# Optimization experiments

Measured on AMD Instinct MI355X. Metric: run time of the kernel, lower is better.

Reference implementation:

```python
import jax, jax.numpy as jnp
import numpy as np

# ---- fixed configuration (from init_kwargs / sensor='WV3', ratio=4) ----
B, NBANDS, H, W = 4, 8, 512, 512
RATIO = 4
BETA = 0.25
KSIZE = 41                    # MTF kernel size used by gen_mtf
SCALE = 2                     # ceil(ratio / 2), StructuralLoss half-window
MASK_HW = 8                   # half-window used by local_corr_mask
MTF_R = MTF_C = 2             # strided scatter offsets in SpectralLossNocorr
EPS = 1e-20
# WV3 Nyquist gains (one per MS band)
GNYQ = np.asarray([0.325, 0.355, 0.360, 0.350, 0.365, 0.360, 0.335, 0.315])


def gen_mtf_kernel():
    """Per-band Gaussian MTF filter, shape (NBANDS, 1, K, K), sum-normalized."""
    fcut = 1.0 / RATIO
    ax = np.arange(KSIZE) - (KSIZE - 1) / 2.0
    xx, yy = np.meshgrid(ax, ax)
    kerns = []
    for g in GNYQ:
        alpha = np.sqrt(((KSIZE - 1) * (fcut / 2.0)) ** 2 / (-2.0 * np.log(g)))
        k = np.exp(-(xx ** 2 + yy ** 2) / (2.0 * alpha ** 2))
        kerns.append(k / k.sum())
    return np.stack(kerns, axis=0)[:, None].astype(np.float32)


def _boxsum(x, w):
    """Sum over a 2w x 2w sliding window via double cumsum (matches torch ref)."""
    x = jnp.pad(x, ((0, 0), (0, 0), (w, w), (w, w)))
    c = jnp.cumsum(jnp.cumsum(x, axis=-1), axis=-2)
    return (c[..., 2 * w:, 2 * w:] - c[..., :-2 * w, 2 * w:]
            - c[..., 2 * w:, :-2 * w] + c[..., :-2 * w, :-2 * w])


def _xcorr(a, b, w):
    """Local cross-correlation (xcorr_torch). a:(B,Ca,H,W), b:(B,Cb,H,W) broadcast."""
    n = 4.0 * w * w
    da = a - _boxsum(a, w) / n
    db = b - _boxsum(b, w) / n
    s_ab = _boxsum(da * db, w)
    s_aa = _boxsum(da * da, w)
    s_bb = _boxsum(db * db, w)
    return s_ab / (jnp.sqrt(s_aa * s_bb) + EPS)


def _depthconv(x, kern):
    # torch Conv2d(groups=nbands, padding='same') == grouped cross-correlation
    return jax.lax.conv_general_dilated(
        x, kern, (1, 1), 'SAME', feature_group_count=kern.shape[0],
        dimension_numbers=('NCHW', 'OIHW', 'NCHW'))


def _local_corr_mask(inp, kern):
    pan = inp[:, -1:, :, :]          # (B,1,H,W)
    ms = inp[:, :-1, :, :]           # (B,NB,H,W)
    k0 = kern[0:1]                   # first-band MTF kernel (1,1,K,K)
    pad = (KSIZE - 1) // 2
    pan = jnp.pad(pan, ((0, 0), (0, 0), (pad, pad), (pad, pad)), mode='edge')
    pan = jax.lax.conv_general_dilated(
        pan, k0, (1, 1), 'VALID', dimension_numbers=('NCHW', 'OIHW', 'NCHW'))
    return 1.0 - _xcorr(pan, ms, MASK_HW)  # (B,NB,H,W)


def setup_inputs() -> dict:
    key = jax.random.key(0)
    k1, k2, k3 = jax.random.split(key, 3)
    return {
        'outputs': jax.random.normal(k1, (B, NBANDS, H, W), jnp.float32),
        'labels': jax.random.uniform(k2, (B, NBANDS + 1, H, W), jnp.float32),
        'inp': jax.random.uniform(k3, (B, NBANDS + 1, H, W), jnp.float32),
        'mtf_kernel': jnp.asarray(gen_mtf_kernel()),           # frozen param
        'spec_mask': jnp.ones((1, NBANDS, H, W), jnp.float32),  # buffer
    }


def reference(outputs, labels, inp, mtf_kernel, spec_mask):
    # ---- SpectralLossNocorr ----
    x = _depthconv(outputs, mtf_kernel)                      # (B,NB,H,W)
    labels_spec = labels[:, :-1]
    sub = labels_spec[:, :, 2::RATIO, 2::RATIO]              # (B,NB,H/4,W/4)
    y = jnp.zeros_like(x).at[:, :, MTF_R::RATIO, MTF_C::RATIO].set(sub)
    msub = jnp.broadcast_to(spec_mask[:, :, 2::RATIO, 2::RATIO], sub.shape)
    Wm = jnp.zeros_like(x).at[:, :, MTF_R::RATIO, MTF_C::RATIO].set(msub)
    Wm = Wm / jnp.sum(Wm)
    L_spec = jnp.sum(jnp.abs(x * Wm - y * Wm))
    # ---- StructuralLoss (with local_corr_mask threshold) ----
    pan = labels[:, -1:, :, :]
    thr = _local_corr_mask(inp, mtf_kernel)                  # (B,NB,H,W)
    Xc = jnp.maximum(_xcorr(outputs, pan, SCALE), -1.0)      # clamp(min=-1)
    X = 1.0 - Xc
    Y = X * (X > thr)                                        # keep worst pixels
    L_struct = jnp.mean(Y)
    return L_spec + BETA * L_struct
```

## Files before the change

kernel.cpp:

```cpp
#include <hip/hip_runtime.h>
#include <hip/hip_bf16.h>

#define HWSZ   262144
#define IMG    512
#define NBATCH 4
#define NBANDS 8

typedef _Float16 half_t;
typedef _Float16 half2v __attribute__((ext_vector_type(2)));
typedef _Float16 half4v __attribute__((ext_vector_type(4)));
typedef _Float16 half8v __attribute__((ext_vector_type(8)));

__device__ __forceinline__ void blockReduceAtomicAdd(double v, double* target,
                                                     double* red) {
    for (int off = 32; off > 0; off >>= 1) v += __shfl_down(v, off, 64);
    const int wave = threadIdx.x >> 6, lane = threadIdx.x & 63;
    if (lane == 0) red[wave] = v;
    __syncthreads();
    if (threadIdx.x == 0) atomicAdd(target, red[0] + red[1] + red[2] + red[3]);
}

__global__ __launch_bounds__(256) void k_pan_h(const float* __restrict__ inp,
                                               const float* __restrict__ mtf,
                                               float* __restrict__ tmpH) {
    __shared__ float seg[296];
    __shared__ float vrow[41];
    const int tid = threadIdx.x;
    const int b = blockIdx.z, r = blockIdx.y, c0 = blockIdx.x * 256;
    if (tid < 41) vrow[tid] = mtf[20 * 41 + tid] / sqrtf(mtf[20 * 41 + 20]);
    const float* pan = inp + ((long)b * 9 + 8) * HWSZ + (long)r * IMG;
    for (int e = tid; e < 296; e += 256) {
        int c = c0 - 20 + e;
        c = min(max(c, 0), IMG - 1);
        seg[e] = pan[c];
    }
    __syncthreads();
    float s = 0.f;
#pragma unroll
    for (int j = 0; j < 41; ++j) s += vrow[j] * seg[tid + j];
    tmpH[(long)b * HWSZ + (long)r * IMG + c0 + tid] = s;
}

__global__ __launch_bounds__(256) void k_pan_v(const float* __restrict__ tmpH,
                                               const float* __restrict__ mtf,
                                               float* __restrict__ panf) {
    __shared__ float ucol[41];
    const int tid = threadIdx.x;
    const int b = blockIdx.z, r = blockIdx.y, c = blockIdx.x * 256 + tid;
    if (tid < 41) ucol[tid] = mtf[tid * 41 + 20] / sqrtf(mtf[20 * 41 + 20]);
    __syncthreads();
    const float* base = tmpH + (long)b * HWSZ;
    float s = 0.f;
#pragma unroll
    for (int i = 0; i < 41; ++i) {
        int rr = min(max(r - 20 + i, 0), IMG - 1);
        s += ucol[i] * base[(long)rr * IMG + c];
    }
    panf[(long)b * HWSZ + (long)r * IMG + c] = s;
}

template <int W>
__global__ __launch_bounds__(256) void k_da(const float* __restrict__ in,
                                            long inBatchStride,
                                            float* __restrict__ out) {
    constexpr int TS = 32, WIN = 2 * W, NN = 4 * W * W, RE = TS + WIN - 1;
    constexpr int SR = RE;
    constexpr int ST = 33;
    __shared__ float RAW[RE * SR];
    __shared__ float T[RE * ST];
    const int tid = threadIdx.x;
    const int tr0 = blockIdx.y * TS, tc0 = blockIdx.x * TS;
    const float* src = in + (long)blockIdx.z * inBatchStride;
    for (int e = tid; e < RE * RE; e += 256) {
        int r = e / RE, c = e % RE;
        int gr = tr0 - (W - 1) + r, gc = tc0 - (W - 1) + c;
        float v = 0.f;
        if (gr >= 0 && gr < IMG && gc >= 0 && gc < IMG) v = src[(long)gr * IMG + gc];
        RAW[r * SR + c] = v;
    }
    __syncthreads();
    for (int e = tid; e < RE * TS; e += 256) {
        int r = e >> 5, j = e & 31;
        float s = 0.f;
#pragma unroll
        for (int k = 0; k < WIN; ++k) s += RAW[r * SR + j + k];
        T[r * ST + j] = s;
    }
    __syncthreads();
    float* dst = out + (long)blockIdx.z * HWSZ;
    for (int e = tid; e < TS * TS; e += 256) {
        int pr = e >> 5, pc = e & 31;
        float s = 0.f;
#pragma unroll
        for (int k = 0; k < WIN; ++k) s += T[(pr + k) * ST + pc];
        float da = RAW[(pr + W - 1) * SR + (pc + W - 1)] - s * (1.0f / NN);
        dst[(long)(tr0 + pr) * IMG + tc0 + pc] = da;
    }
}

template <int W>
__global__ __launch_bounds__(256) void k_sq(const float* __restrict__ in,
                                            float* __restrict__ out) {
    constexpr int TS = 32, WIN = 2 * W, RE = TS + WIN - 1;
    constexpr int SR = RE, ST = 33;
    __shared__ float RAW[RE * SR];
    __shared__ float T[RE * ST];
    const int tid = threadIdx.x;
    const int tr0 = blockIdx.y * TS, tc0 = blockIdx.x * TS;
    const float* src = in + (long)blockIdx.z * HWSZ;
    for (int e = tid; e < RE * RE; e += 256) {
        int r = e / RE, c = e % RE;
        int gr = tr0 - (W - 1) + r, gc = tc0 - (W - 1) + c;
        float v = 0.f;
        if (gr >= 0 && gr < IMG && gc >= 0 && gc < IMG) v = src[(long)gr * IMG + gc];
        RAW[r * SR + c] = v;
    }
    __syncthreads();
    for (int e = tid; e < RE * TS; e += 256) {
        int r = e >> 5, j = e & 31;
        float s = 0.f;
#pragma unroll
        for (int k = 0; k < WIN; ++k) {
            float v = RAW[r * SR + j + k];
            s += v * v;
        }
        T[r * ST + j] = s;
    }
    __syncthreads();
    float* dst = out + (long)blockIdx.z * HWSZ;
    for (int e = tid; e < TS * TS; e += 256) {
        int pr = e >> 5, pc = e & 31;
        float s = 0.f;
#pragma unroll
        for (int k = 0; k < WIN; ++k) s += T[(pr + k) * ST + pc];
        dst[(long)(tr0 + pr) * IMG + tc0 + pc] = s;
    }
}


template <int W> struct WinDims {
    static constexpr int A  = (W + 3) & ~3;
    static constexpr int NU = A + W + 8;
    static constexpr int NF = (NU + 3) / 4;
    static constexpr int NV = NF * 4;
};

template <int W>
__device__ __forceinline__ void loadRowWin(const float* __restrict__ row, int c0,
                                           float* v) {
    constexpr int A = WinDims<W>::A;
    constexpr int NF = WinDims<W>::NF;
#pragma unroll
    for (int f = 0; f < NF; ++f) {
        const int cb = c0 - A + 4 * f;
        if (cb >= 0 && cb + 3 < IMG) {
            const float4 t = *(const float4*)(row + cb);
            v[4 * f + 0] = t.x; v[4 * f + 1] = t.y;
            v[4 * f + 2] = t.z; v[4 * f + 3] = t.w;
        } else {
#pragma unroll
            for (int u = 0; u < 4; ++u) {
                const int c = cb + u;
                v[4 * f + u] = (c >= 0 && c < IMG) ? row[c] : 0.f;
            }
        }
    }
}

template <int W>
__device__ __forceinline__ void loadRowWinH(const half_t* __restrict__ row, int c0,
                                            float* v) {
    constexpr int A = WinDims<W>::A;
    constexpr int NF = WinDims<W>::NF;
#pragma unroll
    for (int f = 0; f < NF; ++f) {
        const int cb = c0 - A + 4 * f;
        if (cb >= 0 && cb + 3 < IMG) {
            const half4v t = *(const half4v*)(row + cb);
            v[4 * f + 0] = (float)t[0]; v[4 * f + 1] = (float)t[1];
            v[4 * f + 2] = (float)t[2]; v[4 * f + 3] = (float)t[3];
        } else {
#pragma unroll
            for (int u = 0; u < 4; ++u) {
                const int c = cb + u;
                v[4 * f + u] = (c >= 0 && c < IMG) ? (float)row[c] : 0.f;
            }
        }
    }
}

template <int W>
__global__ __launch_bounds__(256) void kHbox(const float* __restrict__ in,
                                             long sB, long sC,
                                             half_t* __restrict__ out) {
    constexpr int A = WinDims<W>::A;
    const int g = blockIdx.x * 256 + threadIdx.x;
    const int c0 = (g & 63) << 3, r = (g >> 6) & 511, z = g >> 15;
    const float* row = in + (long)(z >> 3) * sB + (long)(z & 7) * sC + (long)r * IMG;
    float v[WinDims<W>::NV];
    loadRowWin<W>(row, c0, v);
    float o[8];
    float s = 0.f;
#pragma unroll
    for (int i = A - W + 1; i <= A + W; ++i) s += v[i];
    o[0] = s;
#pragma unroll
    for (int j = 1; j < 8; ++j) {
        s += v[A + W + j] - v[A - W + j];
        o[j] = s;
    }
    half8v h;
#pragma unroll
    for (int j = 0; j < 8; ++j) h[j] = (half_t)o[j];
    *(half8v*)(out + (long)z * HWSZ + (long)r * IMG + c0) = h;
}

template <int W>
__global__ __launch_bounds__(256) void kVda(const half_t* __restrict__ t,
                                            const float* __restrict__ orig,
                                            long sB, long sC,
                                            half_t* __restrict__ out) {
    constexpr int NR = 2 * W + 15, NN = 4 * W * W;
    const int g = blockIdx.x * 256 + threadIdx.x;
    const int cp = (g & 255) * 2;
    const int rc = (g >> 8) & 31, z = g >> 13;
    const int r0 = rc * 16;
    const half_t* tz = t + (long)z * HWSZ + cp;
    float vx[NR], vy[NR];
#pragma unroll
    for (int i = 0; i < NR; ++i) {
        const int rr = r0 - W + 1 + i;
        if (rr >= 0 && rr < IMG) {
            const half2v h = *(const half2v*)(tz + (long)rr * IMG);
            vx[i] = (float)h[0]; vy[i] = (float)h[1];
        } else { vx[i] = 0.f; vy[i] = 0.f; }
    }
    const float* oz = orig + (long)(z >> 3) * sB + (long)(z & 7) * sC + cp;
    half_t* dst = out + (long)z * HWSZ + cp;
    float sx = 0.f, sy = 0.f;
#pragma unroll
    for (int i = 0; i < 2 * W; ++i) { sx += vx[i]; sy += vy[i]; }
#pragma unroll
    for (int j = 0; j < 16; ++j) {
        const float2 o = *(const float2*)(oz + (long)(r0 + j) * IMG);
        half2v h;
        h[0] = (half_t)(o.x - sx * (1.0f / NN));
        h[1] = (half_t)(o.y - sy * (1.0f / NN));
        *(half2v*)(dst + (long)(r0 + j) * IMG) = h;
        if (j < 15) {
            sx += vx[2 * W + j] - vx[j];
            sy += vy[2 * W + j] - vy[j];
        }
    }
}

template <int W>
__global__ __launch_bounds__(256) void kHprod(const half_t* __restrict__ da,
                                              const float* __restrict__ dsh,
                                              half_t* __restrict__ o1,
                                              half_t* __restrict__ o2) {
    constexpr int A = WinDims<W>::A;
    constexpr int NU = WinDims<W>::NU;
    constexpr int NV = WinDims<W>::NV;
    const int g = blockIdx.x * 256 + threadIdx.x;
    const int c0 = (g & 63) << 3, r = (g >> 6) & 511, z = g >> 15;
    const half_t* rowa = da + (long)z * HWSZ + (long)r * IMG;
    const float* rows = dsh + (long)(z >> 3) * HWSZ + (long)r * IMG;
    float va[NV], vs[NV];
    loadRowWinH<W>(rowa, c0, va);
    loadRowWin<W>(rows, c0, vs);
    float p1[NV], p2[NV];
#pragma unroll
    for (int i = 0; i < NU; ++i) { p1[i] = va[i] * vs[i]; p2[i] = va[i] * va[i]; }
    float a[8], b[8];
    float s1 = 0.f, s2 = 0.f;
#pragma unroll
    for (int i = A - W + 1; i <= A + W; ++i) { s1 += p1[i]; s2 += p2[i]; }
    a[0] = s1; b[0] = s2;
#pragma unroll
    for (int j = 1; j < 8; ++j) {
        s1 += p1[A + W + j] - p1[A - W + j];
        s2 += p2[A + W + j] - p2[A - W + j];
        a[j] = s1; b[j] = s2;
    }
    half8v h1, h2;
#pragma unroll
    for (int j = 0; j < 8; ++j) { h1[j] = (half_t)a[j]; h2[j] = (half_t)b[j]; }
    *(half8v*)(o1 + (long)z * HWSZ + (long)r * IMG + c0) = h1;
    *(half8v*)(o2 + (long)z * HWSZ + (long)r * IMG + c0) = h2;
}

__global__ __launch_bounds__(256) void kVfinBoth(const half_t* __restrict__ p1,
                                                 const half_t* __restrict__ p2,
                                                 const float* __restrict__ saa,
                                                 const half_t* __restrict__ q1,
                                                 const half_t* __restrict__ q2,
                                                 const float* __restrict__ sbb,
                                                 double* __restrict__ acc) {
    __shared__ double red[4];
    const int g = blockIdx.x * 256 + threadIdx.x;
    const int c = g & 511, rc = (g >> 9) & 31, z = g >> 14;
    const int r0 = rc * 16, b = z >> 3;
    const long zoff = (long)z * HWSZ + c, boff = (long)b * HWSZ + c;

    float thrv[16];
    {
        constexpr int W = 8, NR = 2 * W + 15;
        const half_t* t1 = p1 + zoff;
        const half_t* t2 = p2 + zoff;
        float v1[NR], v2[NR];
#pragma unroll
        for (int i = 0; i < NR; ++i) {
            const int rr = r0 - W + 1 + i;
            const bool ok = (rr >= 0 && rr < IMG);
            v1[i] = ok ? (float)t1[(long)rr * IMG] : 0.f;
            v2[i] = ok ? (float)t2[(long)rr * IMG] : 0.f;
        }
        const float* sz = saa + boff;
        float s1 = 0.f, s2 = 0.f;
#pragma unroll
        for (int i = 0; i < 2 * W; ++i) { s1 += v1[i]; s2 += v2[i]; }
#pragma unroll
        for (int j = 0; j < 16; ++j) {
            const float sa = sz[(long)(r0 + j) * IMG];
            const float den = sqrtf(fmaxf(sa * s2, 0.f)) + 1e-20f;
            thrv[j] = 1.0f - s1 / den;
            if (j < 15) {
                s1 += v1[2 * W + j] - v1[j];
                s2 += v2[2 * W + j] - v2[j];
            }
        }
    }
    double ysum = 0.0;
    {
        constexpr int W = 2, NR = 2 * W + 15;
        const half_t* t1 = q1 + zoff;
        const half_t* t2 = q2 + zoff;
        float v1[NR], v2[NR];
#pragma unroll
        for (int i = 0; i < NR; ++i) {
            const int rr = r0 - W + 1 + i;
            const bool ok = (rr >= 0 && rr < IMG);
            v1[i] = ok ? (float)t1[(long)rr * IMG] : 0.f;
            v2[i] = ok ? (float)t2[(long)rr * IMG] : 0.f;
        }
        const float* sz = sbb + boff;
        float s1 = 0.f, s2 = 0.f;
#pragma unroll
        for (int i = 0; i < 2 * W; ++i) { s1 += v1[i]; s2 += v2[i]; }
#pragma unroll
        for (int j = 0; j < 16; ++j) {
            const float sb = sz[(long)(r0 + j) * IMG];
            const float den = sqrtf(fmaxf(s2 * sb, 0.f)) + 1e-20f;
            const float Xc = s1 / den;
            const float X = 1.0f - fmaxf(Xc, -1.0f);
            if (X > thrv[j]) ysum += (double)X;
            if (j < 15) {
                s1 += v1[2 * W + j] - v1[j];
                s2 += v2[2 * W + j] - v2[j];
            }
        }
    }
    blockReduceAtomicAdd(ysum, acc + 2, red);
}

__global__ __launch_bounds__(256) void k_spec_h(const float* __restrict__ outputs,
                                                const float* __restrict__ mtf,
                                                float* __restrict__ tmpS) {
    __shared__ float vrow[41];
    const int g = blockIdx.x * 256 + threadIdx.x;
    const int q = g & 31, r = (g >> 5) & 511, z = g >> 14;
    const int band = z & 7;
    if (threadIdx.x < 41)
        vrow[threadIdx.x] = mtf[band * 1681 + 20 * 41 + threadIdx.x] /
                            sqrtf(mtf[band * 1681 + 20 * 41 + 20]);
    __syncthreads();
    const float* row = outputs + (long)z * HWSZ + (long)r * IMG;
    float v[56];
#pragma unroll
    for (int f = 0; f < 14; ++f) {
        const int cb = 16 * q - 20 + 4 * f;
        if (cb >= 0 && cb + 3 < IMG) {
            const float4 t = *(const float4*)(row + cb);
            v[4 * f + 0] = t.x; v[4 * f + 1] = t.y;
            v[4 * f + 2] = t.z; v[4 * f + 3] = t.w;
        } else {
#pragma unroll
            for (int u = 0; u < 4; ++u) {
                const int cc = cb + u;
                v[4 * f + u] = (cc >= 0 && cc < IMG) ? row[cc] : 0.f;
            }
        }
    }
    float o[4] = {0.f, 0.f, 0.f, 0.f};
#pragma unroll
    for (int j = 0; j < 41; ++j) {
        const float w = vrow[j];
#pragma unroll
        for (int u = 0; u < 4; ++u) o[u] += w * v[2 + 4 * u + j];
    }
    float* dst = tmpS + ((long)z * IMG + r) * 128 + 4 * q;
    *(float4*)dst = make_float4(o[0], o[1], o[2], o[3]);
}

__global__ __launch_bounds__(256) void k_spec_v(const float* __restrict__ tmpS,
                                                const float* __restrict__ labels,
                                                const float* __restrict__ spec,
                                                const float* __restrict__ mtf,
                                                double* __restrict__ acc) {
    __shared__ double redT[4];
    __shared__ double redM[4];
    __shared__ float ucol[41];
    const int g = blockIdx.x * 256 + threadIdx.x;
    const int q = g & 31, rs = (g >> 5) & 127, z = g >> 12;
    const int b = z >> 3, band = z & 7;
    if (threadIdx.x < 41)
        ucol[threadIdx.x] = mtf[band * 1681 + threadIdx.x * 41 + 20] /
                            sqrtf(mtf[band * 1681 + 20 * 41 + 20]);
    __syncthreads();
    const float* base = tmpS + (long)z * IMG * 128 + 4 * q;
    const int rbase = 4 * rs - 18;
    float o[4] = {0.f, 0.f, 0.f, 0.f};
    if (rbase >= 0 && rbase + 40 < IMG) {
#pragma unroll
        for (int i = 0; i < 41; ++i) {
            const float4 v = *(const float4*)(base + (long)(rbase + i) * 128);
            const float w = ucol[i];
            o[0] += w * v.x; o[1] += w * v.y; o[2] += w * v.z; o[3] += w * v.w;
        }
    } else {
        for (int i = 0; i < 41; ++i) {
            const int r = rbase + i;
            if (r >= 0 && r < IMG) {
                const float4 v = *(const float4*)(base + (long)r * 128);
                const float w = ucol[i];
                o[0] += w * v.x; o[1] += w * v.y; o[2] += w * v.z; o[3] += w * v.w;
            }
        }
    }
    const int gr = 2 + 4 * rs;
    float tsum = 0.f, msum = 0.f;
#pragma unroll
    for (int u = 0; u < 4; ++u) {
        const int gc = 2 + 4 * (4 * q + u);
        const float m = spec[(long)band * HWSZ + (long)gr * IMG + gc];
        const float y = labels[((long)b * 9 + band) * HWSZ + (long)gr * IMG + gc];
        tsum += fabsf(o[u] * m - y * m);
        msum += m;
    }
    blockReduceAtomicAdd((double)tsum, acc + 0, redT);
    blockReduceAtomicAdd((double)msum, acc + 1, redM);
}

__global__ void k_final(const double* __restrict__ acc, float* __restrict__ out) {
    double lspec = acc[0] / acc[1];
    double lstruct = acc[2] / (double)(NBATCH * NBANDS * HWSZ);
    out[0] = (float)(lspec + 0.25 * lstruct);
}

extern "C" void kernel_launch(void* const* d_in, const int* in_sizes, int n_in,
                              void* d_out, int out_size, void* d_ws, size_t ws_size,
                              hipStream_t stream) {
    const float* outputs = (const float*)d_in[0];
    const float* labels  = (const float*)d_in[1];
    const float* inp     = (const float*)d_in[2];
    const float* mtf     = (const float*)d_in[3];
    const float* spec    = (const float*)d_in[4];
    float* out = (float*)d_out;

    const long IMGB = (long)HWSZ;
    char* ws = (char*)d_ws;
    double* acc    = (double*)ws;
    float* panf    = (float*)(ws + 1024);
    float* tmpH    = panf   + NBATCH * IMGB;
    float* da_pan8 = tmpH   + NBATCH * IMGB;
    float* saa8    = da_pan8 + NBATCH * IMGB;
    float* db_pan2 = saa8   + NBATCH * IMGB;
    float* sbb2    = db_pan2 + NBATCH * IMGB;
    float* tmpS    = sbb2   + NBATCH * IMGB;
    half_t* hT     = (half_t*)(tmpS + 8 * IMGB);
    half_t* hDA    = hT  + 32 * IMGB;
    half_t* hP1    = hDA + 32 * IMGB;
    half_t* hP2    = hP1 + 32 * IMGB;
    half_t* hQ1    = hP2 + 32 * IMGB;
    half_t* hQ2    = hQ1 + 32 * IMGB;

    hipMemsetAsync(acc, 0, 4 * sizeof(double), stream);

    k_pan_h<<<dim3(2, 512, NBATCH), 256, 0, stream>>>(inp, mtf, tmpH);
    k_pan_v<<<dim3(2, 512, NBATCH), 256, 0, stream>>>(tmpH, mtf, panf);
    k_da<8><<<dim3(16, 16, NBATCH), 256, 0, stream>>>(panf, (long)HWSZ, da_pan8);
    k_sq<8><<<dim3(16, 16, NBATCH), 256, 0, stream>>>(da_pan8, saa8);
    k_da<2><<<dim3(16, 16, NBATCH), 256, 0, stream>>>(labels + 8 * IMGB,
                                                      (long)9 * HWSZ, db_pan2);
    k_sq<2><<<dim3(16, 16, NBATCH), 256, 0, stream>>>(db_pan2, sbb2);

    k_spec_h<<<2048, 256, 0, stream>>>(outputs, mtf, tmpS);
    k_spec_v<<<512, 256, 0, stream>>>(tmpS, labels, spec, mtf, acc);

    kHbox<8><<<4096, 256, 0, stream>>>(inp, 9 * IMGB, IMGB, hT);
    kVda<8><<<1024, 256, 0, stream>>>(hT, inp, 9 * IMGB, IMGB, hDA);
    kHprod<8><<<4096, 256, 0, stream>>>(hDA, da_pan8, hP1, hP2);

    kHbox<2><<<4096, 256, 0, stream>>>(outputs, 8 * IMGB, IMGB, hT);
    kVda<2><<<1024, 256, 0, stream>>>(hT, outputs, 8 * IMGB, IMGB, hDA);
    kHprod<2><<<4096, 256, 0, stream>>>(hDA, db_pan2, hQ1, hQ2);

    kVfinBoth<<<2048, 256, 0, stream>>>(hP1, hP2, saa8, hQ1, hQ2, sbb2, acc);

    k_final<<<1, 1, 0, stream>>>(acc, out);
}
```

Baseline: 321.0 us.

## Fuse horizontal product boxsums and vertical finalize into one shared-memory tiled kernel

Replaces the two kHprod launches and kVfinBoth with one kernel, kXfused, working on 32x32 tiles. It loads the centred inputs with a halo, forms the products in shared memory, and does both the horizontal and vertical box sums on-chip. This removes the fp16 round trip of the four intermediate product arrays through global memory and saves two launches. In exchange it recomputes the halo (47x47 for the window-8 pass) and uses scalar, non-vectorised global loads and about 35KB of LDS, which may limit occupancy.

```diff
diff --git a/kernel.cpp b/kernel.cpp
--- a/kernel.cpp
+++ b/kernel.cpp
@@ -168,28 +168,6 @@
 }
 
 template <int W>
-__device__ __forceinline__ void loadRowWinH(const half_t* __restrict__ row, int c0,
-                                            float* v) {
-    constexpr int A = WinDims<W>::A;
-    constexpr int NF = WinDims<W>::NF;
-#pragma unroll
-    for (int f = 0; f < NF; ++f) {
-        const int cb = c0 - A + 4 * f;
-        if (cb >= 0 && cb + 3 < IMG) {
-            const half4v t = *(const half4v*)(row + cb);
-            v[4 * f + 0] = (float)t[0]; v[4 * f + 1] = (float)t[1];
-            v[4 * f + 2] = (float)t[2]; v[4 * f + 3] = (float)t[3];
-        } else {
-#pragma unroll
-            for (int u = 0; u < 4; ++u) {
-                const int c = cb + u;
-                v[4 * f + u] = (c >= 0 && c < IMG) ? (float)row[c] : 0.f;
-            }
-        }
-    }
-}
-
-template <int W>
 __global__ __launch_bounds__(256) void kHbox(const float* __restrict__ in,
                                              long sB, long sC,
                                              half_t* __restrict__ out) {
@@ -254,111 +232,119 @@
     }
 }
 
-template <int W>
-__global__ __launch_bounds__(256) void kHprod(const half_t* __restrict__ da,
-                                              const float* __restrict__ dsh,
-                                              half_t* __restrict__ o1,
-                                              half_t* __restrict__ o2) {
-    constexpr int A = WinDims<W>::A;
-    constexpr int NU = WinDims<W>::NU;
-    constexpr int NV = WinDims<W>::NV;
-    const int g = blockIdx.x * 256 + threadIdx.x;
-    const int c0 = (g & 63) << 3, r = (g >> 6) & 511, z = g >> 15;
-    const half_t* rowa = da + (long)z * HWSZ + (long)r * IMG;
-    const float* rows = dsh + (long)(z >> 3) * HWSZ + (long)r * IMG;
-    float va[NV], vs[NV];
-    loadRowWinH<W>(rowa, c0, va);
-    loadRowWin<W>(rows, c0, vs);
-    float p1[NV], p2[NV];
-#pragma unroll
-    for (int i = 0; i < NU; ++i) { p1[i] = va[i] * vs[i]; p2[i] = va[i] * va[i]; }
-    float a[8], b[8];
-    float s1 = 0.f, s2 = 0.f;
-#pragma unroll
-    for (int i = A - W + 1; i <= A + W; ++i) { s1 += p1[i]; s2 += p2[i]; }
-    a[0] = s1; b[0] = s2;
-#pragma unroll
-    for (int j = 1; j < 8; ++j) {
-        s1 += p1[A + W + j] - p1[A - W + j];
-        s2 += p2[A + W + j] - p2[A - W + j];
-        a[j] = s1; b[j] = s2;
-    }
-    half8v h1, h2;
-#pragma unroll
-    for (int j = 0; j < 8; ++j) { h1[j] = (half_t)a[j]; h2[j] = (half_t)b[j]; }
-    *(half8v*)(o1 + (long)z * HWSZ + (long)r * IMG + c0) = h1;
-    *(half8v*)(o2 + (long)z * HWSZ + (long)r * IMG + c0) = h2;
-}
-
-__global__ __launch_bounds__(256) void kVfinBoth(const half_t* __restrict__ p1,
-                                                 const half_t* __restrict__ p2,
-                                                 const float* __restrict__ saa,
-                                                 const half_t* __restrict__ q1,
-                                                 const half_t* __restrict__ q2,
-                                                 const float* __restrict__ sbb,
-                                                 double* __restrict__ acc) {
+__global__ __launch_bounds__(256) void kXfused(
+    const half_t* __restrict__ daMS,
+    const float*  __restrict__ daPAN,
+    const float*  __restrict__ saa,
+    const half_t* __restrict__ daOUT,
+    const float*  __restrict__ dbPAN,
+    const float*  __restrict__ sbb,
+    double* __restrict__ acc) {
+    constexpr int TS = 32;
+    constexpr int RE8 = TS + 15, SR8 = RE8 + 1;
+    constexpr int RE2 = TS + 3,  SR2 = RE2 + 1;
+    constexpr int ST  = TS + 1;
     __shared__ double red[4];
-    const int g = blockIdx.x * 256 + threadIdx.x;
-    const int c = g & 511, rc = (g >> 9) & 31, z = g >> 14;
-    const int r0 = rc * 16, b = z >> 3;
-    const long zoff = (long)z * HWSZ + c, boff = (long)b * HWSZ + c;
-
-    float thrv[16];
+    __shared__ float P1[RE8 * SR8];
+    __shared__ float P2[RE8 * SR8];
+    __shared__ float T1[RE8 * ST];
+    __shared__ float T2[RE8 * ST];
+
+    const int tid = threadIdx.x;
+    const int z = blockIdx.z, b = z >> 3;
+    const int tr0 = blockIdx.y * TS, tc0 = blockIdx.x * TS;
+
+    float thrv[4];
     {
-        constexpr int W = 8, NR = 2 * W + 15;
-        const half_t* t1 = p1 + zoff;
-        const half_t* t2 = p2 + zoff;
-        float v1[NR], v2[NR];
-#pragma unroll
-        for (int i = 0; i < NR; ++i) {
-            const int rr = r0 - W + 1 + i;
-            const bool ok = (rr >= 0 && rr < IMG);
-            v1[i] = ok ? (float)t1[(long)rr * IMG] : 0.f;
-            v2[i] = ok ? (float)t2[(long)rr * IMG] : 0.f;
-        }
-        const float* sz = saa + boff;
-        float s1 = 0.f, s2 = 0.f;
-#pragma unroll
-        for (int i = 0; i < 2 * W; ++i) { s1 += v1[i]; s2 += v2[i]; }
-#pragma unroll
-        for (int j = 0; j < 16; ++j) {
-            const float sa = sz[(long)(r0 + j) * IMG];
+        constexpr int W = 8, RE = RE8, SR = SR8, WIN = 16;
+        const half_t* A = daMS + (long)z * HWSZ;
+        const float*  S = daPAN + (long)b * HWSZ;
+        for (int e = tid; e < RE * RE; e += 256) {
+            const int r = e / RE, c = e % RE;
+            const int gr = tr0 - (W - 1) + r, gc = tc0 - (W - 1) + c;
+            float a = 0.f, s = 0.f;
+            if (gr >= 0 && gr < IMG && gc >= 0 && gc < IMG) {
+                a = (float)A[(long)gr * IMG + gc];
+                s = S[(long)gr * IMG + gc];
+            }
+            P1[r * SR + c] = a * s;
+            P2[r * SR + c] = a * a;
+        }
+        __syncthreads();
+        for (int e = tid; e < RE * TS; e += 256) {
+            const int r = e >> 5, j = e & 31;
+            float s1 = 0.f, s2 = 0.f;
+#pragma unroll
+            for (int k = 0; k < WIN; ++k) {
+                s1 += P1[r * SR + j + k];
+                s2 += P2[r * SR + j + k];
+            }
+            T1[r * ST + j] = s1;
+            T2[r * ST + j] = s2;
+        }
+        __syncthreads();
+        const float* sz = saa + (long)b * HWSZ;
+#pragma unroll
+        for (int k = 0; k < 4; ++k) {
+            const int e = tid + 256 * k;
+            const int pr = e >> 5, pc = e & 31;
+            float s1 = 0.f, s2 = 0.f;
+#pragma unroll
+            for (int kk = 0; kk < WIN; ++kk) {
+                s1 += T1[(pr + kk) * ST + pc];
+                s2 += T2[(pr + kk) * ST + pc];
+            }
+            const float sa = sz[(long)(tr0 + pr) * IMG + tc0 + pc];
             const float den = sqrtf(fmaxf(sa * s2, 0.f)) + 1e-20f;
-            thrv[j] = 1.0f - s1 / den;
-            if (j < 15) {
-                s1 += v1[2 * W + j] - v1[j];
-                s2 += v2[2 * W + j] - v2[j];
-            }
-        }
+            thrv[k] = 1.0f - s1 / den;
+        }
+        __syncthreads();
     }
     double ysum = 0.0;
     {
-        constexpr int W = 2, NR = 2 * W + 15;
-        const half_t* t1 = q1 + zoff;
-        const half_t* t2 = q2 + zoff;
-        float v1[NR], v2[NR];
-#pragma unroll
-        for (int i = 0; i < NR; ++i) {
-            const int rr = r0 - W + 1 + i;
-            const bool ok = (rr >= 0 && rr < IMG);
-            v1[i] = ok ? (float)t1[(long)rr * IMG] : 0.f;
-            v2[i] = ok ? (float)t2[(long)rr * IMG] : 0.f;
-        }
-        const float* sz = sbb + boff;
-        float s1 = 0.f, s2 = 0.f;
-#pragma unroll
-        for (int i = 0; i < 2 * W; ++i) { s1 += v1[i]; s2 += v2[i]; }
-#pragma unroll
-        for (int j = 0; j < 16; ++j) {
-            const float sb = sz[(long)(r0 + j) * IMG];
+        constexpr int W = 2, RE = RE2, SR = SR2, WIN = 4;
+        const half_t* A = daOUT + (long)z * HWSZ;
+        const float*  S = dbPAN + (long)b * HWSZ;
+        for (int e = tid; e < RE * RE; e += 256) {
+            const int r = e / RE, c = e % RE;
+            const int gr = tr0 - (W - 1) + r, gc = tc0 - (W - 1) + c;
+            float a = 0.f, s = 0.f;
+            if (gr >= 0 && gr < IMG && gc >= 0 && gc < IMG) {
+                a = (float)A[(long)gr * IMG + gc];
+                s = S[(long)gr * IMG + gc];
+            }
+            P1[r * SR + c] = a * s;
+            P2[r * SR + c] = a * a;
+        }
+        __syncthreads();
+        for (int e = tid; e < RE * TS; e += 256) {
+            const int r = e >> 5, j = e & 31;
+            float s1 = 0.f, s2 = 0.f;
+#pragma unroll
+            for (int k = 0; k < WIN; ++k) {
+                s1 += P1[r * SR + j + k];
+                s2 += P2[r * SR + j + k];
+            }
+            T1[r * ST + j] = s1;
+            T2[r * ST + j] = s2;
+        }
+        __syncthreads();
+        const float* sz = sbb + (long)b * HWSZ;
+#pragma unroll
+        for (int k = 0; k < 4; ++k) {
+            const int e = tid + 256 * k;
+            const int pr = e >> 5, pc = e & 31;
+            float s1 = 0.f, s2 = 0.f;
+#pragma unroll
+            for (int kk = 0; kk < WIN; ++kk) {
+                s1 += T1[(pr + kk) * ST + pc];
+                s2 += T2[(pr + kk) * ST + pc];
+            }
+            const float sb = sz[(long)(tr0 + pr) * IMG + tc0 + pc];
             const float den = sqrtf(fmaxf(s2 * sb, 0.f)) + 1e-20f;
             const float Xc = s1 / den;
             const float X = 1.0f - fmaxf(Xc, -1.0f);
-            if (X > thrv[j]) ysum += (double)X;
-            if (j < 15) {
-                s1 += v1[2 * W + j] - v1[j];
-                s2 += v2[2 * W + j] - v2[j];
-            }
+            if (X > thrv[k]) ysum += (double)X;
         }
     }
     blockReduceAtomicAdd(ysum, acc + 2, red);
@@ -479,11 +465,8 @@
     float* sbb2    = db_pan2 + NBATCH * IMGB;
     float* tmpS    = sbb2   + NBATCH * IMGB;
     half_t* hT     = (half_t*)(tmpS + 8 * IMGB);
-    half_t* hDA    = hT  + 32 * IMGB;
-    half_t* hP1    = hDA + 32 * IMGB;
-    half_t* hP2    = hP1 + 32 * IMGB;
-    half_t* hQ1    = hP2 + 32 * IMGB;
-    half_t* hQ2    = hQ1 + 32 * IMGB;
+    half_t* hDA8   = hT  + 32 * IMGB;
+    half_t* hDA2   = hDA8 + 32 * IMGB;
 
     hipMemsetAsync(acc, 0, 4 * sizeof(double), stream);
 
@@ -499,14 +482,12 @@
     k_spec_v<<<512, 256, 0, stream>>>(tmpS, labels, spec, mtf, acc);
 
     kHbox<8><<<4096, 256, 0, stream>>>(inp, 9 * IMGB, IMGB, hT);
-    kVda<8><<<1024, 256, 0, stream>>>(hT, inp, 9 * IMGB, IMGB, hDA);
-    kHprod<8><<<4096, 256, 0, stream>>>(hDA, da_pan8, hP1, hP2);
-
+    kVda<8><<<1024, 256, 0, stream>>>(hT, inp, 9 * IMGB, IMGB, hDA8);
     kHbox<2><<<4096, 256, 0, stream>>>(outputs, 8 * IMGB, IMGB, hT);
-    kVda<2><<<1024, 256, 0, stream>>>(hT, outputs, 8 * IMGB, IMGB, hDA);
-    kHprod<2><<<4096, 256, 0, stream>>>(hDA, db_pan2, hQ1, hQ2);
-
-    kVfinBoth<<<2048, 256, 0, stream>>>(hP1, hP2, saa8, hQ1, hQ2, sbb2, acc);
+    kVda<2><<<1024, 256, 0, stream>>>(hT, outputs, 8 * IMGB, IMGB, hDA2);
+
+    kXfused<<<dim3(16, 16, 32), 256, 0, stream>>>(hDA8, da_pan8, saa8,
+                                                  hDA2, db_pan2, sbb2, acc);
 
     k_final<<<1, 1, 0, stream>>>(acc, out);
 }
```

Measured after the change: 361.0 us. 12.5% more time.

## Transpose horizontal box-product outputs so final vertical pass reads rows

Applied to the files above, without the earlier changes.

The horizontal product kernel now stages its results through shared memory and writes them transposed. The squared-sum buffers are also written transposed. The final vertical box pass can then load contiguous rows with the vectorized row-window loader, instead of strided column reads. This swaps strided global reads in the last kernel for an LDS transpose and extra syncs in the product kernel, and it reuses some workspace buffers.

```diff
diff --git a/kernel.cpp b/kernel.cpp
--- a/kernel.cpp
+++ b/kernel.cpp
@@ -100,7 +100,7 @@
 
 template <int W>
 __global__ __launch_bounds__(256) void k_sq(const float* __restrict__ in,
-                                            float* __restrict__ out) {
+                                            float* __restrict__ outT) {
     constexpr int TS = 32, WIN = 2 * W, RE = TS + WIN - 1;
     constexpr int SR = RE, ST = 33;
     __shared__ float RAW[RE * SR];
@@ -127,13 +127,13 @@
         T[r * ST + j] = s;
     }
     __syncthreads();
-    float* dst = out + (long)blockIdx.z * HWSZ;
+    float* dst = outT + (long)blockIdx.z * HWSZ;
     for (int e = tid; e < TS * TS; e += 256) {
-        int pr = e >> 5, pc = e & 31;
+        int pc = e >> 5, pr = e & 31;
         float s = 0.f;
 #pragma unroll
         for (int k = 0; k < WIN; ++k) s += T[(pr + k) * ST + pc];
-        dst[(long)(tr0 + pr) * IMG + tc0 + pc] = s;
+        dst[(long)(tc0 + pc) * IMG + tr0 + pr] = s;
     }
 }
 
@@ -255,109 +255,144 @@
 }
 
 template <int W>
-__global__ __launch_bounds__(256) void kHprod(const half_t* __restrict__ da,
-                                              const float* __restrict__ dsh,
-                                              half_t* __restrict__ o1,
-                                              half_t* __restrict__ o2) {
+__global__ __launch_bounds__(256) void kHprodT(const half_t* __restrict__ da,
+                                               const float* __restrict__ dsh,
+                                               half_t* __restrict__ o1T,
+                                               half_t* __restrict__ o2T) {
     constexpr int A = WinDims<W>::A;
     constexpr int NU = WinDims<W>::NU;
     constexpr int NV = WinDims<W>::NV;
-    const int g = blockIdx.x * 256 + threadIdx.x;
-    const int c0 = (g & 63) << 3, r = (g >> 6) & 511, z = g >> 15;
-    const half_t* rowa = da + (long)z * HWSZ + (long)r * IMG;
-    const float* rows = dsh + (long)(z >> 3) * HWSZ + (long)r * IMG;
-    float va[NV], vs[NV];
-    loadRowWinH<W>(rowa, c0, va);
-    loadRowWin<W>(rows, c0, vs);
-    float p1[NV], p2[NV];
-#pragma unroll
-    for (int i = 0; i < NU; ++i) { p1[i] = va[i] * vs[i]; p2[i] = va[i] * va[i]; }
-    float a[8], b[8];
-    float s1 = 0.f, s2 = 0.f;
-#pragma unroll
-    for (int i = A - W + 1; i <= A + W; ++i) { s1 += p1[i]; s2 += p2[i]; }
-    a[0] = s1; b[0] = s2;
-#pragma unroll
-    for (int j = 1; j < 8; ++j) {
-        s1 += p1[A + W + j] - p1[A - W + j];
-        s2 += p2[A + W + j] - p2[A - W + j];
-        a[j] = s1; b[j] = s2;
-    }
-    half8v h1, h2;
-#pragma unroll
-    for (int j = 0; j < 8; ++j) { h1[j] = (half_t)a[j]; h2[j] = (half_t)b[j]; }
-    *(half8v*)(o1 + (long)z * HWSZ + (long)r * IMG + c0) = h1;
-    *(half8v*)(o2 + (long)z * HWSZ + (long)r * IMG + c0) = h2;
-}
-
-__global__ __launch_bounds__(256) void kVfinBoth(const half_t* __restrict__ p1,
-                                                 const half_t* __restrict__ p2,
-                                                 const float* __restrict__ saa,
-                                                 const half_t* __restrict__ q1,
-                                                 const half_t* __restrict__ q2,
-                                                 const float* __restrict__ sbb,
-                                                 double* __restrict__ acc) {
+    constexpr int LP = 65;
+    __shared__ float L[64 * LP];
+    const int tid = threadIdx.x;
+    const int z = blockIdx.z;
+    const int tr0 = blockIdx.y * 64, tc0 = blockIdx.x * 64;
+    const half_t* daz = da + (long)z * HWSZ;
+    const float* dsz = dsh + (long)(z >> 3) * HWSZ;
+
+    float a[2][8], bb[2][8];
+#pragma unroll
+    for (int u = 0; u < 2; ++u) {
+        const int unit = tid + 256 * u;
+        const int r = unit >> 3, cg = unit & 7;
+        const int gr = tr0 + r, c0 = tc0 + cg * 8;
+        float va[NV], vs[NV];
+        loadRowWinH<W>(daz + (long)gr * IMG, c0, va);
+        loadRowWin<W>(dsz + (long)gr * IMG, c0, vs);
+        float p1[NV], p2[NV];
+#pragma unroll
+        for (int i = 0; i < NU; ++i) { p1[i] = va[i] * vs[i]; p2[i] = va[i] * va[i]; }
+        float s1 = 0.f, s2 = 0.f;
+#pragma unroll
+        for (int i = A - W + 1; i <= A + W; ++i) { s1 += p1[i]; s2 += p2[i]; }
+        a[u][0] = s1; bb[u][0] = s2;
+#pragma unroll
+        for (int j = 1; j < 8; ++j) {
+            s1 += p1[A + W + j] - p1[A - W + j];
+            s2 += p2[A + W + j] - p2[A - W + j];
+            a[u][j] = s1; bb[u][j] = s2;
+        }
+    }
+    const long zbase = (long)z * HWSZ + tr0;
+#pragma unroll
+    for (int u = 0; u < 2; ++u) {
+        const int unit = tid + 256 * u;
+        const int r = unit >> 3, cg = unit & 7;
+#pragma unroll
+        for (int j = 0; j < 8; ++j) L[r * LP + cg * 8 + j] = a[u][j];
+    }
+    __syncthreads();
+#pragma unroll
+    for (int u = 0; u < 2; ++u) {
+        const int e = tid + 256 * u;
+        const int c = e >> 3, r0 = (e & 7) * 8;
+        half8v h;
+#pragma unroll
+        for (int j = 0; j < 8; ++j) h[j] = (half_t)L[(r0 + j) * LP + c];
+        *(half8v*)(o1T + zbase + (long)(tc0 + c) * IMG + r0) = h;
+    }
+    __syncthreads();
+#pragma unroll
+    for (int u = 0; u < 2; ++u) {
+        const int unit = tid + 256 * u;
+        const int r = unit >> 3, cg = unit & 7;
+#pragma unroll
+        for (int j = 0; j < 8; ++j) L[r * LP + cg * 8 + j] = bb[u][j];
+    }
+    __syncthreads();
+#pragma unroll
+    for (int u = 0; u < 2; ++u) {
+        const int e = tid + 256 * u;
+        const int c = e >> 3, r0 = (e & 7) * 8;
+        half8v h;
+#pragma unroll
+        for (int j = 0; j < 8; ++j) h[j] = (half_t)L[(r0 + j) * LP + c];
+        *(half8v*)(o2T + zbase + (long)(tc0 + c) * IMG + r0) = h;
+    }
+}
+
+__global__ __launch_bounds__(256) void kVfinT(const half_t* __restrict__ p1,
+                                              const half_t* __restrict__ p2,
+                                              const float* __restrict__ saaT,
+                                              const half_t* __restrict__ q1,
+                                              const half_t* __restrict__ q2,
+                                              const float* __restrict__ sbbT,
+                                              double* __restrict__ acc) {
     __shared__ double red[4];
     const int g = blockIdx.x * 256 + threadIdx.x;
-    const int c = g & 511, rc = (g >> 9) & 31, z = g >> 14;
-    const int r0 = rc * 16, b = z >> 3;
-    const long zoff = (long)z * HWSZ + c, boff = (long)b * HWSZ + c;
-
-    float thrv[16];
+    const int c0 = (g & 63) << 3;
+    const int rt = (g >> 6) & 511;
+    const int z = g >> 15;
+    const long rowoff = (long)z * HWSZ + (long)rt * IMG;
+    const long soff = (long)(z >> 3) * HWSZ + (long)rt * IMG + c0;
+
+    float thrv[8];
     {
-        constexpr int W = 8, NR = 2 * W + 15;
-        const half_t* t1 = p1 + zoff;
-        const half_t* t2 = p2 + zoff;
-        float v1[NR], v2[NR];
-#pragma unroll
-        for (int i = 0; i < NR; ++i) {
-            const int rr = r0 - W + 1 + i;
-            const bool ok = (rr >= 0 && rr < IMG);
-            v1[i] = ok ? (float)t1[(long)rr * IMG] : 0.f;
-            v2[i] = ok ? (float)t2[(long)rr * IMG] : 0.f;
-        }
-        const float* sz = saa + boff;
+        constexpr int W = 8;
+        constexpr int A = WinDims<W>::A;
+        float v1[WinDims<W>::NV], v2[WinDims<W>::NV];
+        loadRowWinH<W>(p1 + rowoff, c0, v1);
+        loadRowWinH<W>(p2 + rowoff, c0, v2);
+        const float4 sa0 = *(const float4*)(saaT + soff);
+        const float4 sa1 = *(const float4*)(saaT + soff + 4);
+        const float sa[8] = {sa0.x, sa0.y, sa0.z, sa0.w,
+                             sa1.x, sa1.y, sa1.z, sa1.w};
         float s1 = 0.f, s2 = 0.f;
 #pragma unroll
-        for (int i = 0; i < 2 * W; ++i) { s1 += v1[i]; s2 += v2[i]; }
-#pragma unroll
-        for (int j = 0; j < 16; ++j) {
-            const float sa = sz[(long)(r0 + j) * IMG];
-            const float den = sqrtf(fmaxf(sa * s2, 0.f)) + 1e-20f;
+        for (int i = A - W + 1; i <= A + W; ++i) { s1 += v1[i]; s2 += v2[i]; }
+#pragma unroll
+        for (int j = 0; j < 8; ++j) {
+            const float den = sqrtf(fmaxf(sa[j] * s2, 0.f)) + 1e-20f;
             thrv[j] = 1.0f - s1 / den;
-            if (j < 15) {
-                s1 += v1[2 * W + j] - v1[j];
-                s2 += v2[2 * W + j] - v2[j];
+            if (j < 7) {
+                s1 += v1[A + W + 1 + j] - v1[A - W + 1 + j];
+                s2 += v2[A + W + 1 + j] - v2[A - W + 1 + j];
             }
         }
     }
     double ysum = 0.0;
     {
-        constexpr int W = 2, NR = 2 * W + 15;
-        const half_t* t1 = q1 + zoff;
-        const half_t* t2 = q2 + zoff;
-        float v1[NR], v2[NR];
-#pragma unroll
-        for (int i = 0; i < NR; ++i) {
-            const int rr = r0 - W + 1 + i;
-            const bool ok = (rr >= 0 && rr < IMG);
-            v1[i] = ok ? (float)t1[(long)rr * IMG] : 0.f;
-            v2[i] = ok ? (float)t2[(long)rr * IMG] : 0.f;
-        }
-        const float* sz = sbb + boff;
+        constexpr int W = 2;
+        constexpr int A = WinDims<W>::A;
+        float v1[WinDims<W>::NV], v2[WinDims<W>::NV];
+        loadRowWinH<W>(q1 + rowoff, c0, v1);
+        loadRowWinH<W>(q2 + rowoff, c0, v2);
+        const float4 sb0 = *(const float4*)(sbbT + soff);
+        const float4 sb1 = *(const float4*)(sbbT + soff + 4);
+        const float sb[8] = {sb0.x, sb0.y, sb0.z, sb0.w,
+                             sb1.x, sb1.y, sb1.z, sb1.w};
         float s1 = 0.f, s2 = 0.f;
 #pragma unroll
-        for (int i = 0; i < 2 * W; ++i) { s1 += v1[i]; s2 += v2[i]; }
-#pragma unroll
-        for (int j = 0; j < 16; ++j) {
-            const float sb = sz[(long)(r0 + j) * IMG];
-            const float den = sqrtf(fmaxf(s2 * sb, 0.f)) + 1e-20f;
+        for (int i = A - W + 1; i <= A + W; ++i) { s1 += v1[i]; s2 += v2[i]; }
+#pragma unroll
+        for (int j = 0; j < 8; ++j) {
+            const float den = sqrtf(fmaxf(s2 * sb[j], 0.f)) + 1e-20f;
             const float Xc = s1 / den;
             const float X = 1.0f - fmaxf(Xc, -1.0f);
             if (X > thrv[j]) ysum += (double)X;
-            if (j < 15) {
-                s1 += v1[2 * W + j] - v1[j];
-                s2 += v2[2 * W + j] - v2[j];
+            if (j < 7) {
+                s1 += v1[A + W + 1 + j] - v1[A - W + 1 + j];
+                s2 += v2[A + W + 1 + j] - v2[A - W + 1 + j];
             }
         }
     }
@@ -474,39 +509,40 @@
     float* panf    = (float*)(ws + 1024);
     float* tmpH    = panf   + NBATCH * IMGB;
     float* da_pan8 = tmpH   + NBATCH * IMGB;
-    float* saa8    = da_pan8 + NBATCH * IMGB;
-    float* db_pan2 = saa8   + NBATCH * IMGB;
-    float* sbb2    = db_pan2 + NBATCH * IMGB;
-    float* tmpS    = sbb2   + NBATCH * IMGB;
+    float* saaT    = da_pan8 + NBATCH * IMGB;
+    float* db_pan2 = saaT   + NBATCH * IMGB;
+    float* sbbT    = db_pan2 + NBATCH * IMGB;
+    float* tmpS    = sbbT   + NBATCH * IMGB;
     half_t* hT     = (half_t*)(tmpS + 8 * IMGB);
-    half_t* hDA    = hT  + 32 * IMGB;
-    half_t* hP1    = hDA + 32 * IMGB;
-    half_t* hP2    = hP1 + 32 * IMGB;
-    half_t* hQ1    = hP2 + 32 * IMGB;
-    half_t* hQ2    = hQ1 + 32 * IMGB;
+    half_t* hDA8   = hT  + 32 * IMGB;
+    half_t* hDA2   = hDA8 + 32 * IMGB;
+    half_t* hP1T   = hDA2 + 32 * IMGB;
+    half_t* hP2T   = hP1T + 32 * IMGB;
+    half_t* hQ1T   = hDA8;
+    half_t* hQ2T   = hT;
 
     hipMemsetAsync(acc, 0, 4 * sizeof(double), stream);
 
     k_pan_h<<<dim3(2, 512, NBATCH), 256, 0, stream>>>(inp, mtf, tmpH);
     k_pan_v<<<dim3(2, 512, NBATCH), 256, 0, stream>>>(tmpH, mtf, panf);
     k_da<8><<<dim3(16, 16, NBATCH), 256, 0, stream>>>(panf, (long)HWSZ, da_pan8);
-    k_sq<8><<<dim3(16, 16, NBATCH), 256, 0, stream>>>(da_pan8, saa8);
+    k_sq<8><<<dim3(16, 16, NBATCH), 256, 0, stream>>>(da_pan8, saaT);
     k_da<2><<<dim3(16, 16, NBATCH), 256, 0, stream>>>(labels + 8 * IMGB,
                                                       (long)9 * HWSZ, db_pan2);
-    k_sq<2><<<dim3(16, 16, NBATCH), 256, 0, stream>>>(db_pan2, sbb2);
+    k_sq<2><<<dim3(16, 16, NBATCH), 256, 0, stream>>>(db_pan2, sbbT);
 
     k_spec_h<<<2048, 256, 0, stream>>>(outputs, mtf, tmpS);
     k_spec_v<<<512, 256, 0, stream>>>(tmpS, labels, spec, mtf, acc);
 
     kHbox<8><<<4096, 256, 0, stream>>>(inp, 9 * IMGB, IMGB, hT);
-    kVda<8><<<1024, 256, 0, stream>>>(hT, inp, 9 * IMGB, IMGB, hDA);
-    kHprod<8><<<4096, 256, 0, stream>>>(hDA, da_pan8, hP1, hP2);
+    kVda<8><<<1024, 256, 0, stream>>>(hT, inp, 9 * IMGB, IMGB, hDA8);
+    kHprodT<8><<<dim3(8, 8, 32), 256, 0, stream>>>(hDA8, da_pan8, hP1T, hP2T);
 
     kHbox<2><<<4096, 256, 0, stream>>>(outputs, 8 * IMGB, IMGB, hT);
-    kVda<2><<<1024, 256, 0, stream>>>(hT, outputs, 8 * IMGB, IMGB, hDA);
-    kHprod<2><<<4096, 256, 0, stream>>>(hDA, db_pan2, hQ1, hQ2);
-
-    kVfinBoth<<<2048, 256, 0, stream>>>(hP1, hP2, saa8, hQ1, hQ2, sbb2, acc);
+    kVda<2><<<1024, 256, 0, stream>>>(hT, outputs, 8 * IMGB, IMGB, hDA2);
+    kHprodT<2><<<dim3(8, 8, 32), 256, 0, stream>>>(hDA2, db_pan2, hQ1T, hQ2T);
+
+    kVfinT<<<4096, 256, 0, stream>>>(hP1T, hP2T, saaT, hQ1T, hQ2T, sbbT, acc);
 
     k_final<<<1, 1, 0, stream>>>(acc, out);
 }
```

Result: slower. 338.0 us (+5.3%).

## Fuse horizontal product box-sums into vertical pass via shared-memory tiles

Applied to the files above, without the earlier changes.

Replaces the separate kHprod kernels, which wrote two half-precision product box-sum planes per window size, and the combined vertical-finish kernel. The new kFusedThr and kFusedY kernels compute the horizontal products for a 64x64 tile plus halo rows into LDS as packed half2, then do the vertical sliding sum from LDS. The threshold is written as a half plane and read back by the second kernel. This removes the four intermediate half-plane round trips through global memory. The cost is redundant halo-row computation (up to about 25% for W=8), LDS usage that limits occupancy, and an extra half-precision rounding of the threshold.

```diff
diff --git a/kernel.cpp b/kernel.cpp
--- a/kernel.cpp
+++ b/kernel.cpp
@@ -254,111 +254,120 @@
     }
 }
 
-template <int W>
-__global__ __launch_bounds__(256) void kHprod(const half_t* __restrict__ da,
-                                              const float* __restrict__ dsh,
-                                              half_t* __restrict__ o1,
-                                              half_t* __restrict__ o2) {
+
+template <int W>
+__device__ __forceinline__ void stageProducts(const half_t* __restrict__ daz,
+                                              const float* __restrict__ dsz,
+                                              int tr0, int tc0,
+                                              unsigned int* L) {
     constexpr int A = WinDims<W>::A;
     constexpr int NU = WinDims<W>::NU;
     constexpr int NV = WinDims<W>::NV;
-    const int g = blockIdx.x * 256 + threadIdx.x;
-    const int c0 = (g & 63) << 3, r = (g >> 6) & 511, z = g >> 15;
-    const half_t* rowa = da + (long)z * HWSZ + (long)r * IMG;
-    const float* rows = dsh + (long)(z >> 3) * HWSZ + (long)r * IMG;
-    float va[NV], vs[NV];
-    loadRowWinH<W>(rowa, c0, va);
-    loadRowWin<W>(rows, c0, vs);
-    float p1[NV], p2[NV];
-#pragma unroll
-    for (int i = 0; i < NU; ++i) { p1[i] = va[i] * vs[i]; p2[i] = va[i] * va[i]; }
-    float a[8], b[8];
+    constexpr int NRS = 63 + 2 * W;
+    constexpr int LP = 65;
+    for (int e = threadIdx.x; e < NRS * 8; e += 256) {
+        const int i = e >> 3, cg = e & 7;
+        const int gr = tr0 - W + 1 + i;
+        const int c0 = tc0 + cg * 8;
+        unsigned int* dst = L + i * LP + cg * 8;
+        if (gr < 0 || gr >= IMG) {
+#pragma unroll
+            for (int j = 0; j < 8; ++j) dst[j] = 0u;
+            continue;
+        }
+        float va[NV], vs[NV];
+        loadRowWinH<W>(daz + (long)gr * IMG, c0, va);
+        loadRowWin<W>(dsz + (long)gr * IMG, c0, vs);
+        float p1[NV], p2[NV];
+#pragma unroll
+        for (int k = 0; k < NU; ++k) { p1[k] = va[k] * vs[k]; p2[k] = va[k] * va[k]; }
+        float s1 = 0.f, s2 = 0.f;
+#pragma unroll
+        for (int k = A - W + 1; k <= A + W; ++k) { s1 += p1[k]; s2 += p2[k]; }
+#pragma unroll
+        for (int j = 0; j < 8; ++j) {
+            half2v h;
+            h[0] = (half_t)s1; h[1] = (half_t)s2;
+            dst[j] = __builtin_bit_cast(unsigned int, h);
+            if (j < 7) {
+                s1 += p1[A + W + 1 + j] - p1[A - W + 1 + j];
+                s2 += p2[A + W + 1 + j] - p2[A - W + 1 + j];
+            }
+        }
+    }
+}
+
+__global__ __launch_bounds__(256) void kFusedThr(const half_t* __restrict__ daMS,
+                                                 const float* __restrict__ daPAN,
+                                                 const float* __restrict__ saa,
+                                                 half_t* __restrict__ thr) {
+    constexpr int W = 8, LP = 65, NRS = 63 + 2 * W;
+    __shared__ unsigned int L[NRS * LP];
+    const int z = blockIdx.z, b = z >> 3;
+    const int tr0 = blockIdx.y * 64, tc0 = blockIdx.x * 64;
+    stageProducts<W>(daMS + (long)z * HWSZ, daPAN + (long)b * HWSZ, tr0, tc0, L);
+    __syncthreads();
+    const int c = threadIdx.x & 63, q = threadIdx.x >> 6;
+    const int ro0 = q * 16;
     float s1 = 0.f, s2 = 0.f;
 #pragma unroll
-    for (int i = A - W + 1; i <= A + W; ++i) { s1 += p1[i]; s2 += p2[i]; }
-    a[0] = s1; b[0] = s2;
-#pragma unroll
-    for (int j = 1; j < 8; ++j) {
-        s1 += p1[A + W + j] - p1[A - W + j];
-        s2 += p2[A + W + j] - p2[A - W + j];
-        a[j] = s1; b[j] = s2;
-    }
-    half8v h1, h2;
-#pragma unroll
-    for (int j = 0; j < 8; ++j) { h1[j] = (half_t)a[j]; h2[j] = (half_t)b[j]; }
-    *(half8v*)(o1 + (long)z * HWSZ + (long)r * IMG + c0) = h1;
-    *(half8v*)(o2 + (long)z * HWSZ + (long)r * IMG + c0) = h2;
-}
-
-__global__ __launch_bounds__(256) void kVfinBoth(const half_t* __restrict__ p1,
-                                                 const half_t* __restrict__ p2,
-                                                 const float* __restrict__ saa,
-                                                 const half_t* __restrict__ q1,
-                                                 const half_t* __restrict__ q2,
-                                                 const float* __restrict__ sbb,
-                                                 double* __restrict__ acc) {
+    for (int k = 0; k < 2 * W; ++k) {
+        const half2v h = __builtin_bit_cast(half2v, L[(ro0 + k) * LP + c]);
+        s1 += (float)h[0]; s2 += (float)h[1];
+    }
+    const float* sz = saa + (long)b * HWSZ + tc0 + c;
+    half_t* tz = thr + (long)z * HWSZ + tc0 + c;
+#pragma unroll
+    for (int j = 0; j < 16; ++j) {
+        const int r = tr0 + ro0 + j;
+        const float sa = sz[(long)r * IMG];
+        const float den = sqrtf(fmaxf(sa * s2, 0.f)) + 1e-20f;
+        tz[(long)r * IMG] = (half_t)(1.0f - s1 / den);
+        if (j < 15) {
+            const half2v ha = __builtin_bit_cast(half2v, L[(ro0 + j + 2 * W) * LP + c]);
+            const half2v hs = __builtin_bit_cast(half2v, L[(ro0 + j) * LP + c]);
+            s1 += (float)ha[0] - (float)hs[0];
+            s2 += (float)ha[1] - (float)hs[1];
+        }
+    }
+}
+
+__global__ __launch_bounds__(256) void kFusedY(const half_t* __restrict__ daOUT,
+                                               const float* __restrict__ dbPAN,
+                                               const float* __restrict__ sbb,
+                                               const half_t* __restrict__ thr,
+                                               double* __restrict__ acc) {
+    constexpr int W = 2, LP = 65, NRS = 63 + 2 * W;
+    __shared__ unsigned int L[NRS * LP];
     __shared__ double red[4];
-    const int g = blockIdx.x * 256 + threadIdx.x;
-    const int c = g & 511, rc = (g >> 9) & 31, z = g >> 14;
-    const int r0 = rc * 16, b = z >> 3;
-    const long zoff = (long)z * HWSZ + c, boff = (long)b * HWSZ + c;
-
-    float thrv[16];
-    {
-        constexpr int W = 8, NR = 2 * W + 15;
-        const half_t* t1 = p1 + zoff;
-        const half_t* t2 = p2 + zoff;
-        float v1[NR], v2[NR];
-#pragma unroll
-        for (int i = 0; i < NR; ++i) {
-            const int rr = r0 - W + 1 + i;
-            const bool ok = (rr >= 0 && rr < IMG);
-            v1[i] = ok ? (float)t1[(long)rr * IMG] : 0.f;
-            v2[i] = ok ? (float)t2[(long)rr * IMG] : 0.f;
-        }
-        const float* sz = saa + boff;
-        float s1 = 0.f, s2 = 0.f;
-#pragma unroll
-        for (int i = 0; i < 2 * W; ++i) { s1 += v1[i]; s2 += v2[i]; }
-#pragma unroll
-        for (int j = 0; j < 16; ++j) {
-            const float sa = sz[(long)(r0 + j) * IMG];
-            const float den = sqrtf(fmaxf(sa * s2, 0.f)) + 1e-20f;
-            thrv[j] = 1.0f - s1 / den;
-            if (j < 15) {
-                s1 += v1[2 * W + j] - v1[j];
-                s2 += v2[2 * W + j] - v2[j];
-            }
-        }
-    }
+    const int z = blockIdx.z, b = z >> 3;
+    const int tr0 = blockIdx.y * 64, tc0 = blockIdx.x * 64;
+    stageProducts<W>(daOUT + (long)z * HWSZ, dbPAN + (long)b * HWSZ, tr0, tc0, L);
+    __syncthreads();
+    const int c = threadIdx.x & 63, q = threadIdx.x >> 6;
+    const int ro0 = q * 16;
+    float s1 = 0.f, s2 = 0.f;
+#pragma unroll
+    for (int k = 0; k < 2 * W; ++k) {
+        const half2v h = __builtin_bit_cast(half2v, L[(ro0 + k) * LP + c]);
+        s1 += (float)h[0]; s2 += (float)h[1];
+    }
+    const float* sz = sbb + (long)b * HWSZ + tc0 + c;
+    const half_t* tz = thr + (long)z * HWSZ + tc0 + c;
     double ysum = 0.0;
-    {
-        constexpr int W = 2, NR = 2 * W + 15;
-        const half_t* t1 = q1 + zoff;
-        const half_t* t2 = q2 + zoff;
-        float v1[NR], v2[NR];
-#pragma unroll
-        for (int i = 0; i < NR; ++i) {
-            const int rr = r0 - W + 1 + i;
-            const bool ok = (rr >= 0 && rr < IMG);
-            v1[i] = ok ? (float)t1[(long)rr * IMG] : 0.f;
-            v2[i] = ok ? (float)t2[(long)rr * IMG] : 0.f;
-        }
-        const float* sz = sbb + boff;
-        float s1 = 0.f, s2 = 0.f;
-#pragma unroll
-        for (int i = 0; i < 2 * W; ++i) { s1 += v1[i]; s2 += v2[i]; }
-#pragma unroll
-        for (int j = 0; j < 16; ++j) {
-            const float sb = sz[(long)(r0 + j) * IMG];
-            const float den = sqrtf(fmaxf(s2 * sb, 0.f)) + 1e-20f;
-            const float Xc = s1 / den;
-            const float X = 1.0f - fmaxf(Xc, -1.0f);
-            if (X > thrv[j]) ysum += (double)X;
-            if (j < 15) {
-                s1 += v1[2 * W + j] - v1[j];
-                s2 += v2[2 * W + j] - v2[j];
-            }
+#pragma unroll
+    for (int j = 0; j < 16; ++j) {
+        const int r = tr0 + ro0 + j;
+        const float sb = sz[(long)r * IMG];
+        const float den = sqrtf(fmaxf(s2 * sb, 0.f)) + 1e-20f;
+        const float Xc = s1 / den;
+        const float X = 1.0f - fmaxf(Xc, -1.0f);
+        if (X > (float)tz[(long)r * IMG]) ysum += (double)X;
+        if (j < 15) {
+            const half2v ha = __builtin_bit_cast(half2v, L[(ro0 + j + 2 * W) * LP + c]);
+            const half2v hs = __builtin_bit_cast(half2v, L[(ro0 + j) * LP + c]);
+            s1 += (float)ha[0] - (float)hs[0];
+            s2 += (float)ha[1] - (float)hs[1];
         }
     }
     blockReduceAtomicAdd(ysum, acc + 2, red);
@@ -479,11 +488,9 @@
     float* sbb2    = db_pan2 + NBATCH * IMGB;
     float* tmpS    = sbb2   + NBATCH * IMGB;
     half_t* hT     = (half_t*)(tmpS + 8 * IMGB);
-    half_t* hDA    = hT  + 32 * IMGB;
-    half_t* hP1    = hDA + 32 * IMGB;
-    half_t* hP2    = hP1 + 32 * IMGB;
-    half_t* hQ1    = hP2 + 32 * IMGB;
-    half_t* hQ2    = hQ1 + 32 * IMGB;
+    half_t* hDA8   = hT   + 32 * IMGB;
+    half_t* hDA2   = hDA8 + 32 * IMGB;
+    half_t* thrH   = hDA2 + 32 * IMGB;
 
     hipMemsetAsync(acc, 0, 4 * sizeof(double), stream);
 
@@ -499,14 +506,12 @@
     k_spec_v<<<512, 256, 0, stream>>>(tmpS, labels, spec, mtf, acc);
 
     kHbox<8><<<4096, 256, 0, stream>>>(inp, 9 * IMGB, IMGB, hT);
-    kVda<8><<<1024, 256, 0, stream>>>(hT, inp, 9 * IMGB, IMGB, hDA);
-    kHprod<8><<<4096, 256, 0, stream>>>(hDA, da_pan8, hP1, hP2);
-
+    kVda<8><<<1024, 256, 0, stream>>>(hT, inp, 9 * IMGB, IMGB, hDA8);
     kHbox<2><<<4096, 256, 0, stream>>>(outputs, 8 * IMGB, IMGB, hT);
-    kVda<2><<<1024, 256, 0, stream>>>(hT, outputs, 8 * IMGB, IMGB, hDA);
-    kHprod<2><<<4096, 256, 0, stream>>>(hDA, db_pan2, hQ1, hQ2);
-
-    kVfinBoth<<<2048, 256, 0, stream>>>(hP1, hP2, saa8, hQ1, hQ2, sbb2, acc);
+    kVda<2><<<1024, 256, 0, stream>>>(hT, outputs, 8 * IMGB, IMGB, hDA2);
+
+    kFusedThr<<<dim3(8, 8, 32), 256, 0, stream>>>(hDA8, da_pan8, saa8, thrH);
+    kFusedY<<<dim3(8, 8, 32), 256, 0, stream>>>(hDA2, db_pan2, sbb2, thrH, acc);
 
     k_final<<<1, 1, 0, stream>>>(acc, out);
 }
```

New measurement: 312.8 us. -2.6%, faster.
